# Performance work log

Measured on AMD Instinct MI355X. Metric: run time of the kernel, lower is better.

Reference implementation:

```python
import jax, jax.numpy as jnp
import numpy as np

BS, N, H, W, C3D, K = 2, 4096, 64, 192, 64, 3


def _leaky(x):
    return jnp.where(x >= 0, x, 0.1 * x)


def setup_inputs() -> dict:
    key = jax.random.key(0)
    ks = jax.random.split(key, 10)
    # uv: pixel coordinates (x in [0,W), y in [0,H)), channel-first [bs,2,N]
    uv = jax.random.uniform(ks[0], (BS, 2, N), dtype=jnp.float32)
    uv = uv * jnp.array([W, H], dtype=jnp.float32)[None, :, None]
    feat_2d = jax.random.normal(ks[1], (BS, 64, H, W), dtype=jnp.float32)
    feat_3d = jax.random.normal(ks[2], (BS, C3D, N), dtype=jnp.float32)
    w1 = jax.random.normal(ks[3], (16, 3), dtype=jnp.float32) * 0.3
    b1 = jax.random.normal(ks[4], (16,), dtype=jnp.float32) * 0.1
    w2 = jax.random.normal(ks[5], (C3D, 16), dtype=jnp.float32) * 0.2
    b2 = jax.random.normal(ks[6], (C3D,), dtype=jnp.float32) * 0.1
    w_out = jax.random.normal(ks[7], (C3D, C3D), dtype=jnp.float32) * 0.1
    b_out = jax.random.normal(ks[8], (C3D,), dtype=jnp.float32) * 0.1
    return {"uv": uv, "feat_2d": feat_2d, "feat_3d": feat_3d,
            "w1": w1, "b1": b1, "w2": w2, "b2": b2,
            "w_out": w_out, "b_out": b_out}


def reference(uv, feat_2d, feat_3d, w1, b1, w2, b2, w_out, b_out):
    bs, _, image_h, image_w = feat_2d.shape
    c3d = feat_3d.shape[1]
    hw = image_h * image_w

    # mesh grid, channel order (x, y), flattened row-major over (h, w): [bs,2,HW]
    ys, xs = jnp.meshgrid(jnp.arange(image_h, dtype=jnp.float32),
                          jnp.arange(image_w, dtype=jnp.float32), indexing='ij')
    grid = jnp.stack([xs.ravel(), ys.ravel()], axis=0)  # [2, HW]
    grid = jnp.broadcast_to(grid[None], (bs, 2, hw))

    # k-NN of uv points for each grid query: squared distances [bs, HW, N]
    d2 = (jnp.sum(grid * grid, axis=1)[:, :, None]
          + jnp.sum(uv * uv, axis=1)[:, None, :]
          - 2.0 * jnp.einsum('bcq,bcn->bqn', grid, uv))
    _, knn_idx = jax.lax.top_k(-d2, K)  # [bs, HW, K]

    # gather uv and feat_3d by neighbor indices: [bs, 2+C, HW, K]
    data = jnp.concatenate([uv, feat_3d], axis=1)
    knn = jax.vmap(lambda d, i: d[:, i])(data, knn_idx)
    knn_uv, knn_feat3d = knn[:, :2], knn[:, 2:]

    knn_offset = knn_uv - grid[..., None]                      # [bs,2,HW,K]
    offset_norm = jnp.linalg.norm(knn_offset, axis=1, keepdims=True)
    score_in = jnp.concatenate([knn_offset, offset_norm], 1)   # [bs,3,HW,K]

    # score net: 1x1 conv (3->16, leaky_relu 0.1) -> 1x1 conv (16->C, sigmoid)
    h1 = _leaky(jnp.einsum('bcqk,oc->boqk', score_in, w1) + b1[None, :, None, None])
    score = jax.nn.sigmoid(jnp.einsum('bcqk,oc->boqk', h1, w2) + b2[None, :, None, None])

    final = jnp.sum(score * knn_feat3d, axis=-1)               # [bs,C,HW]
    final = final.reshape(bs, c3d, image_h, image_w)

    # out conv: 1x1 conv (C->C) + leaky_relu 0.1
    out = _leaky(jnp.einsum('bchw,oc->bohw', final, w_out) + b_out[None, :, None, None])
    return out
```

## Files before the change

### kernel.cpp

```cpp
#include <hip/hip_runtime.h>
#include <math.h>

#define NBS 2
#define NPTS 4096
#define HH 64
#define WW 192
#define HW (HH*WW)
#define NC 64
#define GX 24
#define GY 8
#define NCELL (GX*GY)

#define FBIG 3.0e38f

__global__ __launch_bounds__(256) void k0_prep(
    const float* __restrict__ uv, const float* __restrict__ f3d,
    float* __restrict__ f3dT, float4* __restrict__ binned,
    int* __restrict__ cellStart) {
#pragma clang fp contract(off)
  int bid = blockIdx.x;
  int t = threadIdx.x;
  if (bid < 128) {
    int b = bid >> 6;
    int nt = (bid & 63) << 6;
    __shared__ float tile[64][65];
    int n_in = t & 63;
    int r0 = t >> 6;
    const float* src = f3d + (size_t)b * NC * NPTS;
#pragma unroll
    for (int r = 0; r < 16; ++r) {
      int c = r0 + (r << 2);
      tile[c][n_in] = src[(size_t)c * NPTS + nt + n_in];
    }
    __syncthreads();
    float* dst = f3dT + ((size_t)b * NPTS + nt) * NC;
    int c_out = t & 63;
#pragma unroll
    for (int r = 0; r < 16; ++r) {
      int n = r0 + (r << 2);
      dst[(size_t)n * NC + c_out] = tile[c_out][n];
    }
  } else {
    int b = bid - 128;
    __shared__ int hist[NCELL + 1];
    __shared__ int cur[NCELL];
    if (t < NCELL + 1) hist[t] = 0;
    __syncthreads();
    const float* u0p = uv + (size_t)b * 2 * NPTS;
    const float* u1p = u0p + NPTS;
    for (int n = t; n < NPTS; n += 256) {
      float u0 = u0p[n], u1 = u1p[n];
      int cxp = min((int)(u0 * 0.125f), GX - 1);
      int cyp = min((int)(u1 * 0.125f), GY - 1);
      atomicAdd(&hist[cyp * GX + cxp + 1], 1);
    }
    __syncthreads();
    if (t == 0) {
      int acc = 0;
      for (int c = 1; c <= NCELL; ++c) { acc += hist[c]; hist[c] = acc; }
    }
    __syncthreads();
    if (t < NCELL) cur[t] = hist[t];
    if (t <= NCELL) cellStart[b * 200 + t] = hist[t];
    __syncthreads();
    for (int n = t; n < NPTS; n += 256) {
      float u0 = u0p[n], u1 = u1p[n];
      float s0 = u0 * u0;
      float s1 = u1 * u1;
      float uu = s0 + s1;
      int cxp = min((int)(u0 * 0.125f), GX - 1);
      int cyp = min((int)(u1 * 0.125f), GY - 1);
      int pos = atomicAdd(&cur[cyp * GX + cxp], 1);
      binned[(size_t)b * NPTS + pos] =
          make_float4(u0 + u0, u1 + u1, uu, __int_as_float(n));
    }
  }
}

__global__ __launch_bounds__(256) void k1_knn(
    const float4* __restrict__ binned, const int* __restrict__ cellStart,
    int4* __restrict__ idxOut) {
#pragma clang fp contract(off)
  int t = threadIdx.x;
  int j = t & 7;
  int qi = blockIdx.x * 32 + (t >> 3);
  int b = blockIdx.y;
  int x = qi % WW, y = qi / WW;
  float xf = (float)x, yf = (float)y;
  float gg = xf * xf + yf * yf;
  int cx = x >> 3, cy = y >> 3;

  const float4* __restrict__ pts = binned + (size_t)b * NPTS;
  const int* __restrict__ cs = cellStart + b * 200;

  float v0 = FBIG, v1 = FBIG, v2 = FBIG;
  int i0 = 0x7FFFFFFF, i1 = 0x7FFFFFFF, i2 = 0x7FFFFFFF;

  auto ins = [&](float d, int gi) {
    bool lt2 = (d < v2) || (d == v2 && gi < i2);
    bool lt1 = (d < v1) || (d == v1 && gi < i1);
    bool lt0 = (d < v0) || (d == v0 && gi < i0);
    i2 = lt1 ? i1 : (lt2 ? gi : i2);
    v2 = lt1 ? v1 : (lt2 ? d : v2);
    i1 = lt0 ? i0 : (lt1 ? gi : i1);
    v1 = lt0 ? v0 : (lt1 ? d : v1);
    i0 = lt0 ? gi : i0;
    v0 = lt0 ? d : v0;
  };
  auto scanRow = [&](int ry, int cA, int cB) {
    int s = cs[ry * GX + cA];
    int e = cs[ry * GX + cB + 1];
    for (int n = s + j; n < e; n += 8) {
      float4 p = pts[n];
      float d = (gg + p.z) - __builtin_fmaf(yf, p.y, xf * p.x);
      ins(d, __float_as_int(p.w));
    }
  };
  auto mergeAll = [&]() {
#pragma unroll
    for (int m = 1; m <= 4; m <<= 1) {
      float ov0 = __shfl_xor(v0, m), ov1 = __shfl_xor(v1, m),
            ov2 = __shfl_xor(v2, m);
      int oi0 = __shfl_xor(i0, m), oi1 = __shfl_xor(i1, m),
          oi2 = __shfl_xor(i2, m);
      ins(ov0, oi0); ins(ov1, oi1); ins(ov2, oi2);
    }
  };

  int cxL = max(cx - 1, 0), cxH = min(cx + 1, GX - 1);
  int cyL = max(cy - 1, 0), cyH = min(cy + 1, GY - 1);
  for (int ry = cyL; ry <= cyH; ++ry) scanRow(ry, cxL, cxH);
  mergeAll();

  while (true) {
    bool fullDom = (cxL == 0 && cxH == GX - 1 && cyL == 0 && cyH == GY - 1);
    float dL = (cxL > 0) ? (xf - (float)(cxL * 8)) : FBIG;
    float dR = (cxH < GX - 1) ? ((float)((cxH + 1) * 8) - xf) : FBIG;
    float dB = (cyL > 0) ? (yf - (float)(cyL * 8)) : FBIG;
    float dT = (cyH < GY - 1) ? ((float)((cyH + 1) * 8) - yf) : FBIG;
    float dmin = fminf(fminf(dL, dR), fminf(dB, dT));
    if (fullDom || (v2 < dmin * dmin - 4.0f)) break;
    int nxL = max(cxL - 1, 0), nxH = min(cxH + 1, GX - 1);
    int nyL = max(cyL - 1, 0), nyH = min(cyH + 1, GY - 1);
    for (int ry = nyL; ry <= nyH; ++ry) {
      if (ry < cyL || ry > cyH) scanRow(ry, nxL, nxH);
      else {
        if (nxL < cxL) scanRow(ry, nxL, cxL - 1);
        if (nxH > cxH) scanRow(ry, cxH + 1, nxH);
      }
    }
    cxL = nxL; cxH = nxH; cyL = nyL; cyH = nyH;
    mergeAll();
  }

  if (j == 0) idxOut[(size_t)b * HW + qi] = make_int4(i0, i1, i2, 0);
}

__global__ __launch_bounds__(256) void k2b_mlp(
    const int4* __restrict__ idx4, const float* __restrict__ uv,
    const float* __restrict__ f3dT,
    const float* __restrict__ w1, const float* __restrict__ b1,
    const float* __restrict__ w2, const float* __restrict__ b2,
    const float* __restrict__ w_out, const float* __restrict__ b_out,
    float* __restrict__ out) {
  int blk = blockIdx.x;
  int b = blockIdx.y;
  int t = threadIdx.x;
  int ql = t & 15;
  int cg = t >> 4;
  int q = blk * 16 + ql;
  float xf = (float)(q % WW);
  float yf = (float)(q / WW);

  int4 id4 = idx4[(size_t)b * HW + q];
  int idx[3] = {id4.x, id4.y, id4.z};

  float h1a[3][16];
#pragma unroll
  for (int k = 0; k < 3; ++k) {
    int i = idx[k];
    float u0 = uv[(size_t)b * 2 * NPTS + i];
    float u1 = uv[(size_t)b * 2 * NPTS + NPTS + i];
    float dx = u0 - xf;
    float dy = u1 - yf;
    float nrm = sqrtf(dx * dx + dy * dy);
#pragma unroll
    for (int o = 0; o < 16; ++o) {
      float h = fmaf(w1[o * 3 + 0], dx,
               fmaf(w1[o * 3 + 1], dy,
               fmaf(w1[o * 3 + 2], nrm, b1[o])));
      h1a[k][o] = (h >= 0.0f) ? h : 0.1f * h;
    }
  }

  __shared__ float fin[16][65];

  {
    float4 f0 = *(const float4*)(f3dT + ((size_t)b * NPTS + idx[0]) * NC + cg * 4);
    float4 f1 = *(const float4*)(f3dT + ((size_t)b * NPTS + idx[1]) * NC + cg * 4);
    float4 f2 = *(const float4*)(f3dT + ((size_t)b * NPTS + idx[2]) * NC + cg * 4);
    float fa[4] = {f0.x, f0.y, f0.z, f0.w};
    float fb[4] = {f1.x, f1.y, f1.z, f1.w};
    float fc[4] = {f2.x, f2.y, f2.z, f2.w};
#pragma unroll
    for (int cc = 0; cc < 4; ++cc) {
      int c = cg * 4 + cc;
      float bias = b2[c];
      float s0 = bias, s1 = bias, s2 = bias;
#pragma unroll
      for (int o = 0; o < 16; ++o) {
        float wv = w2[c * 16 + o];
        s0 = fmaf(wv, h1a[0][o], s0);
        s1 = fmaf(wv, h1a[1][o], s1);
        s2 = fmaf(wv, h1a[2][o], s2);
      }
      float g0 = 1.0f / (1.0f + __expf(-s0));
      float g1 = 1.0f / (1.0f + __expf(-s1));
      float g2 = 1.0f / (1.0f + __expf(-s2));
      fin[ql][c] = g0 * fa[cc] + g1 * fb[cc] + g2 * fc[cc];
    }
  }
  __syncthreads();

  int o0 = cg * 4;
  float acc[4];
#pragma unroll
  for (int jj = 0; jj < 4; ++jj) acc[jj] = b_out[o0 + jj];
  for (int c = 0; c < 64; ++c) {
    float f = fin[ql][c];
#pragma unroll
    for (int jj = 0; jj < 4; ++jj)
      acc[jj] = fmaf(w_out[(o0 + jj) * 64 + c], f, acc[jj]);
  }
  float* dst = out + ((size_t)(b * 64 + o0)) * HW + q;
#pragma unroll
  for (int jj = 0; jj < 4; ++jj) {
    float v = acc[jj];
    dst[(size_t)jj * HW] = (v >= 0.0f) ? v : 0.1f * v;
  }
}

extern "C" void kernel_launch(void* const* d_in, const int* in_sizes, int n_in,
                              void* d_out, int out_size, void* d_ws, size_t ws_size,
                              hipStream_t stream) {
  const float* uv   = (const float*)d_in[0];
  const float* f3d  = (const float*)d_in[2];
  const float* w1   = (const float*)d_in[3];
  const float* b1   = (const float*)d_in[4];
  const float* w2   = (const float*)d_in[5];
  const float* b2   = (const float*)d_in[6];
  const float* wout = (const float*)d_in[7];
  const float* bout = (const float*)d_in[8];
  float* out = (float*)d_out;

  char* ws = (char*)d_ws;
  float*  f3dT      = (float*)(ws);
  float4* binned    = (float4*)(ws + 2097152);
  int*    cellStart = (int*)(ws + 2228224);
  int4*   idx4      = (int4*)(ws + 2232320);

  hipLaunchKernelGGL(k0_prep, dim3(130), dim3(256), 0, stream,
                     uv, f3d, f3dT, binned, cellStart);
  hipLaunchKernelGGL(k1_knn, dim3(HW / 32, NBS), dim3(256), 0, stream,
                     (const float4*)binned, (const int*)cellStart, idx4);
  hipLaunchKernelGGL(k2b_mlp, dim3(HW / 16, NBS), dim3(256), 0, stream,
                     (const int4*)idx4, uv, f3dT, w1, b1, w2, b2, wout, bout, out);
}
```

Measured before the change: 52.85 us.

## Fuse kNN search and score MLP into one kernel, parallelize prefix scan

```diff
diff --git a/kernel.cpp b/kernel.cpp
--- a/kernel.cpp
+++ b/kernel.cpp
@@ -44,7 +44,7 @@
     int b = bid - 128;
     __shared__ int hist[NCELL + 1];
     __shared__ int cur[NCELL];
-    if (t < NCELL + 1) hist[t] = 0;
+    if (t <= NCELL) hist[t] = 0;
     __syncthreads();
     const float* u0p = uv + (size_t)b * 2 * NPTS;
     const float* u1p = u0p + NPTS;
@@ -55,11 +55,13 @@
       atomicAdd(&hist[cyp * GX + cxp + 1], 1);
     }
     __syncthreads();
-    if (t == 0) {
-      int acc = 0;
-      for (int c = 1; c <= NCELL; ++c) { acc += hist[c]; hist[c] = acc; }
-    }
-    __syncthreads();
+    for (int off = 1; off <= NCELL; off <<= 1) {
+      int v = 0;
+      if (t <= NCELL && t >= off) v = hist[t - off];
+      __syncthreads();
+      if (t <= NCELL && t >= off) hist[t] += v;
+      __syncthreads();
+    }
     if (t < NCELL) cur[t] = hist[t];
     if (t <= NCELL) cellStart[b * 200 + t] = hist[t];
     __syncthreads();
@@ -77,103 +79,102 @@
   }
 }
 
-__global__ __launch_bounds__(256) void k1_knn(
+__global__ __launch_bounds__(256) void k_main(
     const float4* __restrict__ binned, const int* __restrict__ cellStart,
-    int4* __restrict__ idxOut) {
-#pragma clang fp contract(off)
-  int t = threadIdx.x;
-  int j = t & 7;
-  int qi = blockIdx.x * 32 + (t >> 3);
-  int b = blockIdx.y;
-  int x = qi % WW, y = qi / WW;
-  float xf = (float)x, yf = (float)y;
-  float gg = xf * xf + yf * yf;
-  int cx = x >> 3, cy = y >> 3;
-
-  const float4* __restrict__ pts = binned + (size_t)b * NPTS;
-  const int* __restrict__ cs = cellStart + b * 200;
-
-  float v0 = FBIG, v1 = FBIG, v2 = FBIG;
-  int i0 = 0x7FFFFFFF, i1 = 0x7FFFFFFF, i2 = 0x7FFFFFFF;
-
-  auto ins = [&](float d, int gi) {
-    bool lt2 = (d < v2) || (d == v2 && gi < i2);
-    bool lt1 = (d < v1) || (d == v1 && gi < i1);
-    bool lt0 = (d < v0) || (d == v0 && gi < i0);
-    i2 = lt1 ? i1 : (lt2 ? gi : i2);
-    v2 = lt1 ? v1 : (lt2 ? d : v2);
-    i1 = lt0 ? i0 : (lt1 ? gi : i1);
-    v1 = lt0 ? v0 : (lt1 ? d : v1);
-    i0 = lt0 ? gi : i0;
-    v0 = lt0 ? d : v0;
-  };
-  auto scanRow = [&](int ry, int cA, int cB) {
-    int s = cs[ry * GX + cA];
-    int e = cs[ry * GX + cB + 1];
-    for (int n = s + j; n < e; n += 8) {
-      float4 p = pts[n];
-      float d = (gg + p.z) - __builtin_fmaf(yf, p.y, xf * p.x);
-      ins(d, __float_as_int(p.w));
-    }
-  };
-  auto mergeAll = [&]() {
-#pragma unroll
-    for (int m = 1; m <= 4; m <<= 1) {
-      float ov0 = __shfl_xor(v0, m), ov1 = __shfl_xor(v1, m),
-            ov2 = __shfl_xor(v2, m);
-      int oi0 = __shfl_xor(i0, m), oi1 = __shfl_xor(i1, m),
-          oi2 = __shfl_xor(i2, m);
-      ins(ov0, oi0); ins(ov1, oi1); ins(ov2, oi2);
-    }
-  };
-
-  int cxL = max(cx - 1, 0), cxH = min(cx + 1, GX - 1);
-  int cyL = max(cy - 1, 0), cyH = min(cy + 1, GY - 1);
-  for (int ry = cyL; ry <= cyH; ++ry) scanRow(ry, cxL, cxH);
-  mergeAll();
-
-  while (true) {
-    bool fullDom = (cxL == 0 && cxH == GX - 1 && cyL == 0 && cyH == GY - 1);
-    float dL = (cxL > 0) ? (xf - (float)(cxL * 8)) : FBIG;
-    float dR = (cxH < GX - 1) ? ((float)((cxH + 1) * 8) - xf) : FBIG;
-    float dB = (cyL > 0) ? (yf - (float)(cyL * 8)) : FBIG;
-    float dT = (cyH < GY - 1) ? ((float)((cyH + 1) * 8) - yf) : FBIG;
-    float dmin = fminf(fminf(dL, dR), fminf(dB, dT));
-    if (fullDom || (v2 < dmin * dmin - 4.0f)) break;
-    int nxL = max(cxL - 1, 0), nxH = min(cxH + 1, GX - 1);
-    int nyL = max(cyL - 1, 0), nyH = min(cyH + 1, GY - 1);
-    for (int ry = nyL; ry <= nyH; ++ry) {
-      if (ry < cyL || ry > cyH) scanRow(ry, nxL, nxH);
-      else {
-        if (nxL < cxL) scanRow(ry, nxL, cxL - 1);
-        if (nxH > cxH) scanRow(ry, cxH + 1, nxH);
-      }
-    }
-    cxL = nxL; cxH = nxH; cyL = nyL; cyH = nyH;
-    mergeAll();
-  }
-
-  if (j == 0) idxOut[(size_t)b * HW + qi] = make_int4(i0, i1, i2, 0);
-}
-
-__global__ __launch_bounds__(256) void k2b_mlp(
-    const int4* __restrict__ idx4, const float* __restrict__ uv,
-    const float* __restrict__ f3dT,
+    const float* __restrict__ uv, const float* __restrict__ f3dT,
     const float* __restrict__ w1, const float* __restrict__ b1,
     const float* __restrict__ w2, const float* __restrict__ b2,
     const float* __restrict__ w_out, const float* __restrict__ b_out,
     float* __restrict__ out) {
-  int blk = blockIdx.x;
+#pragma clang fp contract(off)
+  int t = threadIdx.x;
   int b = blockIdx.y;
-  int t = threadIdx.x;
+
+  __shared__ int sidx[16][4];
+  __shared__ float fin[16][68];
+
+  {
+    int Q = t >> 4;
+    int j = t & 15;
+    int qi = blockIdx.x * 16 + Q;
+    int x = qi % WW, y = qi / WW;
+    float xf = (float)x, yf = (float)y;
+    float gg = xf * xf + yf * yf;
+    int cx = x >> 3, cy = y >> 3;
+
+    const float4* __restrict__ pts = binned + (size_t)b * NPTS;
+    const int* __restrict__ cs = cellStart + b * 200;
+
+    float v0 = FBIG, v1 = FBIG, v2 = FBIG;
+    int i0 = 0x7FFFFFFF, i1 = 0x7FFFFFFF, i2 = 0x7FFFFFFF;
+
+    auto ins = [&](float d, int gi) {
+      bool lt2 = (d < v2) || (d == v2 && gi < i2);
+      bool lt1 = (d < v1) || (d == v1 && gi < i1);
+      bool lt0 = (d < v0) || (d == v0 && gi < i0);
+      i2 = lt1 ? i1 : (lt2 ? gi : i2);
+      v2 = lt1 ? v1 : (lt2 ? d : v2);
+      i1 = lt0 ? i0 : (lt1 ? gi : i1);
+      v1 = lt0 ? v0 : (lt1 ? d : v1);
+      i0 = lt0 ? gi : i0;
+      v0 = lt0 ? d : v0;
+    };
+    auto scanRow = [&](int ry, int cA, int cB) {
+      int s = cs[ry * GX + cA];
+      int e = cs[ry * GX + cB + 1];
+      for (int n = s + j; n < e; n += 16) {
+        float4 p = pts[n];
+        float d = (gg + p.z) - __builtin_fmaf(yf, p.y, xf * p.x);
+        ins(d, __float_as_int(p.w));
+      }
+    };
+    auto mergeAll = [&]() {
+#pragma unroll
+      for (int m = 1; m <= 8; m <<= 1) {
+        float ov0 = __shfl_xor(v0, m), ov1 = __shfl_xor(v1, m),
+              ov2 = __shfl_xor(v2, m);
+        int oi0 = __shfl_xor(i0, m), oi1 = __shfl_xor(i1, m),
+            oi2 = __shfl_xor(i2, m);
+        ins(ov0, oi0); ins(ov1, oi1); ins(ov2, oi2);
+      }
+    };
+
+    int cxL = max(cx - 1, 0), cxH = min(cx + 1, GX - 1);
+    int cyL = max(cy - 1, 0), cyH = min(cy + 1, GY - 1);
+    for (int ry = cyL; ry <= cyH; ++ry) scanRow(ry, cxL, cxH);
+    mergeAll();
+
+    while (true) {
+      bool fullDom = (cxL == 0 && cxH == GX - 1 && cyL == 0 && cyH == GY - 1);
+      float dL = (cxL > 0) ? (xf - (float)(cxL * 8)) : FBIG;
+      float dR = (cxH < GX - 1) ? ((float)((cxH + 1) * 8) - xf) : FBIG;
+      float dB = (cyL > 0) ? (yf - (float)(cyL * 8)) : FBIG;
+      float dT = (cyH < GY - 1) ? ((float)((cyH + 1) * 8) - yf) : FBIG;
+      float dmin = fminf(fminf(dL, dR), fminf(dB, dT));
+      if (fullDom || (v2 < dmin * dmin - 4.0f)) break;
+      int nxL = max(cxL - 1, 0), nxH = min(cxH + 1, GX - 1);
+      int nyL = max(cyL - 1, 0), nyH = min(cyH + 1, GY - 1);
+      for (int ry = nyL; ry <= nyH; ++ry) {
+        if (ry < cyL || ry > cyH) scanRow(ry, nxL, nxH);
+        else {
+          if (nxL < cxL) scanRow(ry, nxL, cxL - 1);
+          if (nxH > cxH) scanRow(ry, cxH + 1, nxH);
+        }
+      }
+      cxL = nxL; cxH = nxH; cyL = nyL; cyH = nyH;
+      mergeAll();
+    }
+
+    if (j == 0) { sidx[Q][0] = i0; sidx[Q][1] = i1; sidx[Q][2] = i2; }
+  }
+  __syncthreads();
+
   int ql = t & 15;
   int cg = t >> 4;
-  int q = blk * 16 + ql;
+  int q = blockIdx.x * 16 + ql;
   float xf = (float)(q % WW);
   float yf = (float)(q / WW);
-
-  int4 id4 = idx4[(size_t)b * HW + q];
-  int idx[3] = {id4.x, id4.y, id4.z};
+  int idx[3] = {sidx[ql][0], sidx[ql][1], sidx[ql][2]};
 
   float h1a[3][16];
 #pragma unroll
@@ -183,7 +184,7 @@
     float u1 = uv[(size_t)b * 2 * NPTS + NPTS + i];
     float dx = u0 - xf;
     float dy = u1 - yf;
-    float nrm = sqrtf(dx * dx + dy * dy);
+    float nrm = sqrtf(__builtin_fmaf(dx, dx, dy * dy));
 #pragma unroll
     for (int o = 0; o < 16; ++o) {
       float h = fmaf(w1[o * 3 + 0], dx,
@@ -192,8 +193,6 @@
       h1a[k][o] = (h >= 0.0f) ? h : 0.1f * h;
     }
   }
-
-  __shared__ float fin[16][65];
 
   {
     float4 f0 = *(const float4*)(f3dT + ((size_t)b * NPTS + idx[0]) * NC + cg * 4);
@@ -207,17 +206,23 @@
       int c = cg * 4 + cc;
       float bias = b2[c];
       float s0 = bias, s1 = bias, s2 = bias;
-#pragma unroll
-      for (int o = 0; o < 16; ++o) {
-        float wv = w2[c * 16 + o];
-        s0 = fmaf(wv, h1a[0][o], s0);
-        s1 = fmaf(wv, h1a[1][o], s1);
-        s2 = fmaf(wv, h1a[2][o], s2);
+      const float4* w2r = (const float4*)(w2 + c * 16);
+#pragma unroll
+      for (int o4 = 0; o4 < 4; ++o4) {
+        float4 wv = w2r[o4];
+        float wvs[4] = {wv.x, wv.y, wv.z, wv.w};
+#pragma unroll
+        for (int oo = 0; oo < 4; ++oo) {
+          int o = o4 * 4 + oo;
+          s0 = fmaf(wvs[oo], h1a[0][o], s0);
+          s1 = fmaf(wvs[oo], h1a[1][o], s1);
+          s2 = fmaf(wvs[oo], h1a[2][o], s2);
+        }
       }
       float g0 = 1.0f / (1.0f + __expf(-s0));
       float g1 = 1.0f / (1.0f + __expf(-s1));
       float g2 = 1.0f / (1.0f + __expf(-s2));
-      fin[ql][c] = g0 * fa[cc] + g1 * fb[cc] + g2 * fc[cc];
+      fin[ql][c] = fmaf(g0, fa[cc], fmaf(g1, fb[cc], g2 * fc[cc]));
     }
   }
   __syncthreads();
@@ -226,11 +231,18 @@
   float acc[4];
 #pragma unroll
   for (int jj = 0; jj < 4; ++jj) acc[jj] = b_out[o0 + jj];
-  for (int c = 0; c < 64; ++c) {
-    float f = fin[ql][c];
-#pragma unroll
-    for (int jj = 0; jj < 4; ++jj)
-      acc[jj] = fmaf(w_out[(o0 + jj) * 64 + c], f, acc[jj]);
+  const float4* finq = (const float4*)(&fin[ql][0]);
+#pragma unroll 4
+  for (int c4 = 0; c4 < 16; ++c4) {
+    float4 f = finq[c4];
+#pragma unroll
+    for (int jj = 0; jj < 4; ++jj) {
+      float4 wv = *(const float4*)(w_out + (o0 + jj) * 64 + c4 * 4);
+      acc[jj] = fmaf(wv.x, f.x,
+                fmaf(wv.y, f.y,
+                fmaf(wv.z, f.z,
+                fmaf(wv.w, f.w, acc[jj]))));
+    }
   }
   float* dst = out + ((size_t)(b * 64 + o0)) * HW + q;
 #pragma unroll
@@ -257,12 +269,10 @@
   float*  f3dT      = (float*)(ws);
   float4* binned    = (float4*)(ws + 2097152);
   int*    cellStart = (int*)(ws + 2228224);
-  int4*   idx4      = (int4*)(ws + 2232320);
 
   hipLaunchKernelGGL(k0_prep, dim3(130), dim3(256), 0, stream,
                      uv, f3d, f3dT, binned, cellStart);
-  hipLaunchKernelGGL(k1_knn, dim3(HW / 32, NBS), dim3(256), 0, stream,
-                     (const float4*)binned, (const int*)cellStart, idx4);
-  hipLaunchKernelGGL(k2b_mlp, dim3(HW / 16, NBS), dim3(256), 0, stream,
-                     (const int4*)idx4, uv, f3dT, w1, b1, w2, b2, wout, bout, out);
+  hipLaunchKernelGGL(k_main, dim3(HW / 16, NBS), dim3(256), 0, stream,
+                     (const float4*)binned, (const int*)cellStart,
+                     uv, f3dT, w1, b1, w2, b2, wout, bout, out);
 }
```

New measurement: 50.49 us. -4.5%, faster.
